# Kernel optimization log

Measured on AMD Instinct MI355X. Metric: run time of the kernel, lower is better.

Reference implementation:

```python
import jax, jax.numpy as jnp
import numpy as np

D_MODEL = 256
D_STATE = 64
NGROUPS = 2
EXPAND = 4
HEADDIM = 128
D_CONV = 4
D_INNER = EXPAND * D_MODEL              # 1024
NHEADS = D_INNER // HEADDIM             # 8
GN = NGROUPS * D_STATE                  # 128
D_IN_PROJ = 2 * D_INNER + 2 * GN + NHEADS  # 2312
EPS = 1e-5


def setup_inputs() -> dict:
    key = jax.random.key(0)
    ks = jax.random.split(key, 12)
    B, L = 2, 4096
    u = jax.random.normal(ks[0], (B, L, D_MODEL), dtype=jnp.float32)
    ln_gamma = jnp.ones((D_MODEL,), jnp.float32)
    ln_beta = jnp.zeros((D_MODEL,), jnp.float32)
    W_in = jax.random.normal(ks[1], (D_MODEL, D_IN_PROJ), jnp.float32) / np.sqrt(D_MODEL)
    conv_w = jax.random.normal(ks[2], (D_INNER + 2 * GN, D_CONV), jnp.float32) * 0.2
    conv_b = jax.random.normal(ks[3], (D_INNER + 2 * GN,), jnp.float32) * 0.02
    dt_bias = jnp.log(jnp.expm1(jax.random.uniform(ks[4], (NHEADS,), jnp.float32, 0.001, 0.1)))
    A_log = jnp.log(jax.random.uniform(ks[5], (NHEADS,), jnp.float32, 1.0, 16.0))
    D_param = jnp.ones((NHEADS,), jnp.float32)
    B_head_scale = jnp.ones((NHEADS, GN), jnp.float32) + 0.02 * jax.random.normal(ks[6], (NHEADS, GN), jnp.float32)
    rms_weight = jnp.ones((D_INNER,), jnp.float32)
    W_out = jax.random.normal(ks[7], (D_INNER, D_MODEL), jnp.float32) / np.sqrt(D_INNER)
    return dict(u=u, ln_gamma=ln_gamma, ln_beta=ln_beta, W_in=W_in, conv_w=conv_w,
                conv_b=conv_b, dt_bias=dt_bias, A_log=A_log, D_param=D_param,
                B_head_scale=B_head_scale, rms_weight=rms_weight, W_out=W_out)


def _mamba_mes(xn, W_in, conv_w, conv_b, dt_bias, A_log, D_param, B_head_scale, rms_weight, W_out):
    B, L, _ = xn.shape
    H, P, K = NHEADS, HEADDIM, D_CONV
    zxbcdt = xn @ W_in                                   # (B,L,2312)
    z = zxbcdt[..., :D_INNER]
    xBC = zxbcdt[..., D_INNER:D_INNER + D_INNER + 2 * GN]
    dt = zxbcdt[..., -H:]
    dt_pos = jax.nn.softplus(dt + dt_bias)               # (B,L,H)
    # causal depthwise conv1d + silu
    xp = jnp.pad(xBC, ((0, 0), (K - 1, 0), (0, 0)))
    conv = sum(xp[:, k:k + L, :] * conv_w[:, k] for k in range(K)) + conv_b
    xBC = jax.nn.silu(conv)
    x = xBC[..., :D_INNER]
    B_shared = xBC[..., D_INNER:D_INNER + GN]            # (B,L,GN)
    C_shared = xBC[..., D_INNER + GN:]                   # (B,L,GN)
    # MES: per-head B via diagonal scale, shared x (mean over heads) and shared C
    B_h = B_shared[:, :, None, :] * B_head_scale[None, None]          # (B,L,H,GN)
    x_shared = x.reshape(B, L, H, P).mean(axis=2)                     # (B,L,P)
    A = -jnp.exp(A_log)                                               # (H,)
    dA = jnp.exp(dt_pos * A)                                          # (B,L,H)
    # selective scan; per-head state (GN, P)
    def step(state, inp):
        dA_t, dt_t, B_t, C_t, x_t = inp   # (B,H),(B,H),(B,H,GN),(B,GN),(B,P)
        state = dA_t[:, :, None, None] * state + jnp.einsum('bh,bhn,bp->bhnp', dt_t, B_t, x_t)
        y_t = jnp.einsum('bn,bhnp->bhp', C_t, state)
        return state, y_t
    init = jnp.zeros((B, H, GN, P), xn.dtype)
    xs = (jnp.moveaxis(dA, 1, 0), jnp.moveaxis(dt_pos, 1, 0), jnp.moveaxis(B_h, 1, 0),
          jnp.moveaxis(C_shared, 1, 0), jnp.moveaxis(x_shared, 1, 0))
    _, ys = jax.lax.scan(step, init, xs)
    y = jnp.moveaxis(ys, 0, 1)                                        # (B,L,H,P)
    y = y + D_param[None, None, :, None] * x_shared[:, :, None, :]    # skip term D*x
    y = y.reshape(B, L, D_INNER)
    # gated RMSNorm: y * silu(z), then rmsnorm
    yg = y * jax.nn.silu(z)
    y = yg * jax.lax.rsqrt(jnp.mean(yg * yg, axis=-1, keepdims=True) + EPS) * rms_weight
    return y @ W_out


def reference(u, ln_gamma, ln_beta, W_in, conv_w, conv_b, dt_bias, A_log,
              D_param, B_head_scale, rms_weight, W_out):
    # pre-LayerNorm
    mu = jnp.mean(u, axis=-1, keepdims=True)
    var = jnp.mean((u - mu) ** 2, axis=-1, keepdims=True)
    xn = (u - mu) * jax.lax.rsqrt(var + EPS) * ln_gamma + ln_beta
    out = _mamba_mes(xn, W_in, conv_w, conv_b, dt_bias, A_log, D_param,
                     B_head_scale, rms_weight, W_out)
    return u + out  # dropout is identity in eval
```

## Files before the change

### kernel.cpp

```cpp
#include <hip/hip_runtime.h>
#include <math.h>

#define LN_TOK 4096
#define NB 2
#define NROWS (NB * LN_TOK)
#define DMODEL 256
#define DINNER 1024
#define NHEADS 8
#define GNN 128
#define DPROJ 2312
#define ZSTRIDE 2432
#define EPSF 1e-5f
#define NCHUNK 32
#define CHUNK 128
#define GPAD 72
#define TT 16

typedef unsigned short u16;
typedef unsigned int u32;
typedef __attribute__((ext_vector_type(8))) short shortx8;
typedef __attribute__((ext_vector_type(4))) float floatx4;

__device__ __forceinline__ float sigmoidf_(float v) { return 1.f / (1.f + __expf(-v)); }
__device__ __forceinline__ float siluf_(float v)    { return v / (1.f + __expf(-v)); }
__device__ __forceinline__ float softplusf_(float v){ return v > 20.f ? v : log1pf(__expf(v)); }
__device__ __forceinline__ float b2f(u16 h) { return __uint_as_float(((u32)h) << 16); }
__device__ __forceinline__ u16 f2b(float f) {
    u32 u = __float_as_uint(f);
    u32 r = (u + 0x7fffu + ((u >> 16) & 1u)) >> 16;
    return (u16)r;
}

__global__ void k_ln(const float* __restrict__ u, const float* __restrict__ gam,
                     const float* __restrict__ bet, u16* __restrict__ xn) {
    int row = blockIdx.x;
    int tid = threadIdx.x;
    float v = u[(size_t)row * DMODEL + tid];
    __shared__ float s1[256], s2[256];
    s1[tid] = v; s2[tid] = v * v;
    __syncthreads();
    for (int off = 128; off > 0; off >>= 1) {
        if (tid < off) { s1[tid] += s1[tid + off]; s2[tid] += s2[tid + off]; }
        __syncthreads();
    }
    float mean = s1[0] * (1.f / DMODEL);
    float var  = s2[0] * (1.f / DMODEL) - mean * mean;
    float r = rsqrtf(var + EPSF);
    xn[(size_t)row * DMODEL + tid] = f2b((v - mean) * r * gam[tid] + bet[tid]);
}

__global__ void k_tcast(const float* __restrict__ in, u16* __restrict__ out,
                        int R, int C, int Cp) {
    __shared__ float tile[64][65];
    int c0 = blockIdx.x * 64, r0 = blockIdx.y * 64;
    int tx = threadIdx.x & 63, ty = threadIdx.x >> 6;
    for (int rr = ty; rr < 64; rr += 4) {
        int r = r0 + rr, c = c0 + tx;
        tile[rr][tx] = (r < R && c < C) ? in[(size_t)r * C + c] : 0.f;
    }
    __syncthreads();
    for (int cc = ty; cc < 64; cc += 4) {
        int c = c0 + cc, r = r0 + tx;
        if (c < Cp && r < R) out[(size_t)c * R + r] = f2b(tile[tx][cc]);
    }
}

__global__ __launch_bounds__(256) void k_gemm_bf(const u16* __restrict__ A,
                                                 const u16* __restrict__ Bt,
                                                 u16* __restrict__ C,
                                                 int K, int ldc) {
    __shared__ u16 As[128 * GPAD];
    __shared__ u16 Bs[128 * GPAD];
    int tid = threadIdx.x;
    int wave = tid >> 6, lane = tid & 63;
    int wm = wave >> 1, wn = wave & 1;
    int quad = lane >> 4, l16 = lane & 15;
    int m0 = blockIdx.y * 128, n0 = blockIdx.x * 128;
    floatx4 acc[4][4] = {};
    for (int k0 = 0; k0 < K; k0 += 64) {
#pragma unroll
        for (int p = 0; p < 4; p++) {
            int i = p * 256 + tid;
            int row = i >> 3, kk = (i & 7) << 3;
            *(int4*)&As[row * GPAD + kk] = *(const int4*)&A[(size_t)(m0 + row) * K + k0 + kk];
            *(int4*)&Bs[row * GPAD + kk] = *(const int4*)&Bt[(size_t)(n0 + row) * K + k0 + kk];
        }
        __syncthreads();
#pragma unroll
        for (int ks = 0; ks < 64; ks += 32) {
            shortx8 af[4], bfr[4];
#pragma unroll
            for (int i = 0; i < 4; i++)
                af[i] = *(shortx8*)&As[(wm * 64 + i * 16 + l16) * GPAD + ks + (quad << 3)];
#pragma unroll
            for (int j = 0; j < 4; j++)
                bfr[j] = *(shortx8*)&Bs[(wn * 64 + j * 16 + l16) * GPAD + ks + (quad << 3)];
#pragma unroll
            for (int i = 0; i < 4; i++)
#pragma unroll
                for (int j = 0; j < 4; j++)
                    acc[i][j] = __builtin_amdgcn_mfma_f32_16x16x32_bf16(af[i], bfr[j], acc[i][j], 0, 0, 0);
        }
        __syncthreads();
    }
#pragma unroll
    for (int i = 0; i < 4; i++) {
        int row = m0 + wm * 64 + i * 16 + quad * 4;
#pragma unroll
        for (int j = 0; j < 4; j++) {
            int col = n0 + wn * 64 + j * 16 + l16;
#pragma unroll
            for (int r = 0; r < 4; r++)
                C[(size_t)(row + r) * ldc + col] = f2b(acc[i][j][r]);
        }
    }
}

__global__ __launch_bounds__(256) void k_gemm2(const u16* __restrict__ A,
                                               const u16* __restrict__ Bt,
                                               float* __restrict__ C,
                                               int K, int ldc,
                                               const float* __restrict__ addC) {
    __shared__ u16 As[128 * GPAD];
    __shared__ u16 Bs[64 * GPAD];
    int tid = threadIdx.x;
    int wave = tid >> 6, lane = tid & 63;
    int wm = wave >> 1, wn = wave & 1;
    int quad = lane >> 4, l16 = lane & 15;
    int m0 = blockIdx.y * 128, n0 = blockIdx.x * 64;
    floatx4 acc[4][2] = {};
    for (int k0 = 0; k0 < K; k0 += 64) {
#pragma unroll
        for (int p = 0; p < 4; p++) {
            int i = p * 256 + tid;
            int row = i >> 3, kk = (i & 7) << 3;
            *(int4*)&As[row * GPAD + kk] = *(const int4*)&A[(size_t)(m0 + row) * K + k0 + kk];
        }
#pragma unroll
        for (int p = 0; p < 2; p++) {
            int i = p * 256 + tid;
            int row = i >> 3, kk = (i & 7) << 3;
            *(int4*)&Bs[row * GPAD + kk] = *(const int4*)&Bt[(size_t)(n0 + row) * K + k0 + kk];
        }
        __syncthreads();
#pragma unroll
        for (int ks = 0; ks < 64; ks += 32) {
            shortx8 af[4], bfr[2];
#pragma unroll
            for (int i = 0; i < 4; i++)
                af[i] = *(shortx8*)&As[(wm * 64 + i * 16 + l16) * GPAD + ks + (quad << 3)];
#pragma unroll
            for (int j = 0; j < 2; j++)
                bfr[j] = *(shortx8*)&Bs[(wn * 32 + j * 16 + l16) * GPAD + ks + (quad << 3)];
#pragma unroll
            for (int i = 0; i < 4; i++)
#pragma unroll
                for (int j = 0; j < 2; j++)
                    acc[i][j] = __builtin_amdgcn_mfma_f32_16x16x32_bf16(af[i], bfr[j], acc[i][j], 0, 0, 0);
        }
        __syncthreads();
    }
#pragma unroll
    for (int i = 0; i < 4; i++) {
        int row = m0 + wm * 64 + i * 16 + quad * 4;
#pragma unroll
        for (int j = 0; j < 2; j++) {
            int col = n0 + wn * 32 + j * 16 + l16;
#pragma unroll
            for (int r = 0; r < 4; r++) {
                size_t idx = (size_t)(row + r) * ldc + col;
                float v = acc[i][j][r];
                if (addC) v += addC[idx];
                C[idx] = v;
            }
        }
    }
}

#define LDW 1296
__global__ __launch_bounds__(256) void k_conv(const u16* __restrict__ zxb,
                                              const float* __restrict__ cw,
                                              const float* __restrict__ cb,
                                              const float* __restrict__ dt_bias,
                                              const float* __restrict__ A_log,
                                              u16* __restrict__ xsh, u16* __restrict__ Bsh,
                                              u16* __restrict__ Csh, u16* __restrict__ XT,
                                              u16* __restrict__ BT,
                                              float* __restrict__ dtp, float* __restrict__ laa) {
    int blk = blockIdx.x;
    int b = blk / (LN_TOK / TT), tile = blk % (LN_TOK / TT);
    int t0 = tile * TT;
    int tid = threadIdx.x;
    __shared__ u16 ld[(TT + 3) * LDW];
    __shared__ float sv[TT][260];
    __shared__ u16 bcv[TT][132];

    for (int i = tid; i < (TT + 3) * 161; i += 256) {
        int r = i / 161, ch = (i % 161) * 8;
        int t = t0 - 3 + r;
        int4 v = make_int4(0, 0, 0, 0);
        if (t >= 0)
            v = *(const int4*)&zxb[((size_t)(b * LN_TOK + t)) * ZSTRIDE + DINNER + ch];
        *(int4*)&ld[r * LDW + ch] = v;
    }

    int cmap[5];
#pragma unroll
    for (int k = 0; k < 4; k++) cmap[k] = (tid >> 7) * 512 + (tid & 127) + 128 * k;
    cmap[4] = 1024 + tid;
    float w0[5], w1[5], w2[5], w3[5], bias[5];
#pragma unroll
    for (int k = 0; k < 5; k++) {
        int c = cmap[k];
        w0[k] = cw[c * 4 + 0]; w1[k] = cw[c * 4 + 1];
        w2[k] = cw[c * 4 + 2]; w3[k] = cw[c * 4 + 3];
        bias[k] = cb[c];
    }
    float dtb = 0.f, negA = 0.f;
    if (tid < NHEADS) { dtb = dt_bias[tid]; negA = -__expf(A_log[tid]); }

    __syncthreads();

    float h1[5], h2[5], h3[5];
#pragma unroll
    for (int k = 0; k < 5; k++) {
        h3[k] = b2f(ld[0 * LDW + cmap[k]]);
        h2[k] = b2f(ld[1 * LDW + cmap[k]]);
        h1[k] = b2f(ld[2 * LDW + cmap[k]]);
    }

    for (int m = 0; m < TT; m++) {
        int t = t0 + m;
        size_t rowp = (size_t)(b * LN_TOK + t) * GNN;
        float xpart = 0.f;
#pragma unroll
        for (int k = 0; k < 5; k++) {
            float cur = b2f(ld[(m + 3) * LDW + cmap[k]]);
            float conv = bias[k] + w3[k] * cur + w2[k] * h1[k] + w1[k] * h2[k] + w0[k] * h3[k];
            h3[k] = h2[k]; h2[k] = h1[k]; h1[k] = cur;
            float s = siluf_(conv);
            if (k < 4) xpart += s;
            else {
                u16 sb = f2b(s);
                if (tid < 128) { Bsh[rowp + tid] = sb; bcv[m][tid] = sb; }
                else           Csh[rowp + tid - 128] = sb;
            }
        }
        sv[m][tid] = xpart;
        if (tid < NHEADS) {
            float dtv = b2f(ld[(m + 3) * LDW + 1280 + tid]) + dtb;
            float dp = softplusf_(dtv);
            size_t idx = ((size_t)(b * NHEADS + tid)) * LN_TOK + t;
            dtp[idx] = dp;
            laa[idx] = negA * dp;
        }
    }
    __syncthreads();

    for (int idx = tid; idx < TT * 128; idx += 256) {
        int m = idx >> 7, p = idx & 127;
        xsh[(size_t)(b * LN_TOK + t0 + m) * GNN + p] =
            f2b((sv[m][p] + sv[m][p + 128]) * 0.125f);
    }
    {
        int p = tid & 127, tg = tid >> 7;
        u16 ox[8], ob[8];
#pragma unroll
        for (int j = 0; j < 8; j++) {
            int m = tg * 8 + j;
            ox[j] = f2b((sv[m][p] + sv[m][p + 128]) * 0.125f);
            ob[j] = bcv[m][p];
        }
        size_t base = ((size_t)(b * GNN + p)) * LN_TOK + t0 + tg * 8;
        int4 vx = make_int4((u32)ox[0] | ((u32)ox[1] << 16), (u32)ox[2] | ((u32)ox[3] << 16),
                            (u32)ox[4] | ((u32)ox[5] << 16), (u32)ox[6] | ((u32)ox[7] << 16));
        int4 vb = make_int4((u32)ob[0] | ((u32)ob[1] << 16), (u32)ob[2] | ((u32)ob[3] << 16),
                            (u32)ob[4] | ((u32)ob[5] << 16), (u32)ob[6] | ((u32)ob[7] << 16));
        *(int4*)&XT[base] = vx;
        *(int4*)&BT[base] = vb;
    }
}

__global__ void k_prefix(const float* __restrict__ laa, float* __restrict__ gcum) {
    int blk = blockIdx.x;
    int bh = blk / NCHUNK, c = blk % NCHUNK;
    int tid = threadIdx.x;
    __shared__ float s[128];
    size_t base = (size_t)bh * LN_TOK + c * CHUNK;
    s[tid] = laa[base + tid];
    __syncthreads();
    for (int off = 1; off < 128; off <<= 1) {
        float v = (tid >= off) ? s[tid - off] : 0.f;
        __syncthreads();
        s[tid] += v;
        __syncthreads();
    }
    gcum[base + tid] = s[tid];
}

__global__ __launch_bounds__(256) void k_chunkM(const u16* __restrict__ Bsh,
                                                const u16* __restrict__ Csh,
                                                const float* __restrict__ scale,
                                                const float* __restrict__ gcum,
                                                const float* __restrict__ dtp,
                                                u16* __restrict__ Mb) {
    int blk = blockIdx.x;
    int c = blk & 31, h = (blk >> 5) & 7, b = blk >> 8;
    int t0 = c * CHUNK;
    __shared__ u16 As[128 * GPAD];
    __shared__ u16 Bs[128 * GPAD];
    __shared__ float g[128], dts[128], sc[128];
    int tid = threadIdx.x;
    int wave = tid >> 6, lane = tid & 63;
    int wm = wave >> 1, wn = wave & 1;
    int quad = lane >> 4, l16 = lane & 15;
    size_t bhbase = (size_t)(b * NHEADS + h) * LN_TOK + t0;
    if (tid < 128) {
        g[tid] = gcum[bhbase + tid];
        dts[tid] = dtp[bhbase + tid];
        sc[tid] = scale[h * GNN + tid];
    }
    __syncthreads();
    floatx4 acc[4][4] = {};
    size_t rbase = (size_t)(b * LN_TOK + t0) * GNN;
    for (int k0 = 0; k0 < 128; k0 += 64) {
#pragma unroll
        for (int p = 0; p < 4; p++) {
            int i = p * 256 + tid;
            int row = i >> 3, kk = (i & 7) << 3;
            int4 raw = *(const int4*)&Bsh[rbase + (size_t)row * GNN + k0 + kk];
            u16* rp = (u16*)&raw;
            u32 w[4];
#pragma unroll
            for (int q = 0; q < 4; q++) {
                u16 a  = f2b(b2f(rp[2 * q])     * sc[k0 + kk + 2 * q]);
                u16 bb = f2b(b2f(rp[2 * q + 1]) * sc[k0 + kk + 2 * q + 1]);
                w[q] = (u32)a | ((u32)bb << 16);
            }
            *(int4*)&As[row * GPAD + kk] = make_int4(w[0], w[1], w[2], w[3]);
            *(int4*)&Bs[row * GPAD + kk] = *(const int4*)&Csh[rbase + (size_t)row * GNN + k0 + kk];
        }
        __syncthreads();
#pragma unroll
        for (int ks = 0; ks < 64; ks += 32) {
            shortx8 af[4], bfr[4];
#pragma unroll
            for (int i = 0; i < 4; i++)
                af[i] = *(shortx8*)&As[(wm * 64 + i * 16 + l16) * GPAD + ks + (quad << 3)];
#pragma unroll
            for (int j = 0; j < 4; j++)
                bfr[j] = *(shortx8*)&Bs[(wn * 64 + j * 16 + l16) * GPAD + ks + (quad << 3)];
#pragma unroll
            for (int i = 0; i < 4; i++)
#pragma unroll
                for (int j = 0; j < 4; j++)
                    acc[i][j] = __builtin_amdgcn_mfma_f32_16x16x32_bf16(af[i], bfr[j], acc[i][j], 0, 0, 0);
        }
        __syncthreads();
    }
    size_t mb = (size_t)blk * (CHUNK * CHUNK);
#pragma unroll
    for (int i = 0; i < 4; i++) {
        int s0 = wm * 64 + i * 16 + quad * 4;
#pragma unroll
        for (int j = 0; j < 4; j++) {
            int t = wn * 64 + j * 16 + l16;
            u16 o[4];
#pragma unroll
            for (int r = 0; r < 4; r++) {
                int s = s0 + r;
                float v = (s <= t) ? acc[i][j][r] * __expf(g[t] - g[s]) * dts[s] : 0.f;
                o[r] = f2b(v);
            }
            u32 lo = (u32)o[0] | ((u32)o[1] << 16);
            u32 hi = (u32)o[2] | ((u32)o[3] << 16);
            *(uint2*)&Mb[mb + (size_t)t * CHUNK + s0] = make_uint2(lo, hi);
        }
    }
}

__global__ __launch_bounds__(256) void k_chunkS(const u16* __restrict__ BT,
                                                const u16* __restrict__ XT,
                                                const float* __restrict__ scale,
                                                const float* __restrict__ gcum,
                                                const float* __restrict__ dtp,
                                                u16* __restrict__ states) {
    int blk = blockIdx.x;
    int c = blk & 31, h = (blk >> 5) & 7, b = blk >> 8;
    int t0 = c * CHUNK;
    __shared__ u16 As[128 * GPAD];
    __shared__ u16 Bs[128 * GPAD];
    __shared__ float esc[128], scl[128];
    int tid = threadIdx.x;
    int wave = tid >> 6, lane = tid & 63;
    int wm = wave >> 1, wn = wave & 1;
    int quad = lane >> 4, l16 = lane & 15;
    size_t bhbase = (size_t)(b * NHEADS + h) * LN_TOK + t0;
    if (tid < 128) {
        float gl = gcum[bhbase + 127];
        esc[tid] = __expf(gl - gcum[bhbase + tid]) * dtp[bhbase + tid];
        scl[tid] = scale[h * GNN + tid];
    }
    __syncthreads();
    floatx4 acc[4][4] = {};
    size_t tbase = (size_t)(b * GNN) * LN_TOK + t0;
    for (int k0 = 0; k0 < 128; k0 += 64) {
#pragma unroll
        for (int p = 0; p < 4; p++) {
            int i = p * 256 + tid;
            int row = i >> 3, kk = (i & 7) << 3;
            int4 raw = *(const int4*)&BT[tbase + (size_t)row * LN_TOK + k0 + kk];
            u16* rp = (u16*)&raw;
            float sr = scl[row];
            u32 w[4];
#pragma unroll
            for (int q = 0; q < 4; q++) {
                u16 a  = f2b(b2f(rp[2 * q])     * sr * esc[k0 + kk + 2 * q]);
                u16 bb = f2b(b2f(rp[2 * q + 1]) * sr * esc[k0 + kk + 2 * q + 1]);
                w[q] = (u32)a | ((u32)bb << 16);
            }
            *(int4*)&As[row * GPAD + kk] = make_int4(w[0], w[1], w[2], w[3]);
            *(int4*)&Bs[row * GPAD + kk] = *(const int4*)&XT[tbase + (size_t)row * LN_TOK + k0 + kk];
        }
        __syncthreads();
#pragma unroll
        for (int ks = 0; ks < 64; ks += 32) {
            shortx8 af[4], bfr[4];
#pragma unroll
            for (int i = 0; i < 4; i++)
                af[i] = *(shortx8*)&As[(wm * 64 + i * 16 + l16) * GPAD + ks + (quad << 3)];
#pragma unroll
            for (int j = 0; j < 4; j++)
                bfr[j] = *(shortx8*)&Bs[(wn * 64 + j * 16 + l16) * GPAD + ks + (quad << 3)];
#pragma unroll
            for (int i = 0; i < 4; i++)
#pragma unroll
                for (int j = 0; j < 4; j++)
                    acc[i][j] = __builtin_amdgcn_mfma_f32_16x16x32_bf16(af[i], bfr[j], acc[i][j], 0, 0, 0);
        }
        __syncthreads();
    }
    size_t sbase = (size_t)blk * 16384;
#pragma unroll
    for (int i = 0; i < 4; i++) {
        int n0 = wm * 64 + i * 16 + quad * 4;
#pragma unroll
        for (int j = 0; j < 4; j++) {
            int p = wn * 64 + j * 16 + l16;
            u16 o[4];
#pragma unroll
            for (int r = 0; r < 4; r++) o[r] = f2b(acc[i][j][r]);
            u32 lo = (u32)o[0] | ((u32)o[1] << 16);
            u32 hi = (u32)o[2] | ((u32)o[3] << 16);
            *(uint2*)&states[sbase + (size_t)p * CHUNK + n0] = make_uint2(lo, hi);
        }
    }
}

__global__ void k_scan(u16* __restrict__ states, const float* __restrict__ gcum) {
    int idx = blockIdx.x * 256 + threadIdx.x;
    int bh = idx >> 14;
    int np = idx & 16383;
    float run = 0.f;
    size_t base = (size_t)bh * NCHUNK * 16384 + np;
    size_t gb = (size_t)bh * LN_TOK;
    for (int c = 0; c < NCHUNK; c++) {
        float G = __expf(gcum[gb + c * CHUNK + 127]);
        float l = b2f(states[base + (size_t)c * 16384]);
        states[base + (size_t)c * 16384] = f2b(run);
        run = G * run + l;
    }
}

__global__ __launch_bounds__(256) void k_chunkY(const u16* __restrict__ Csh,
                                                const u16* __restrict__ states,
                                                const u16* __restrict__ Mb,
                                                const u16* __restrict__ XT,
                                                const float* __restrict__ gcum,
                                                u16* __restrict__ y) {
    int blk = blockIdx.x;
    int c = blk & 31, h = (blk >> 5) & 7, b = blk >> 8;
    int t0 = c * CHUNK;
    __shared__ u16 As[128 * GPAD];
    __shared__ u16 Bs[128 * GPAD];
    __shared__ float eg[128];
    int tid = threadIdx.x;
    int wave = tid >> 6, lane = tid & 63;
    int wm = wave >> 1, wn = wave & 1;
    int quad = lane >> 4, l16 = lane & 15;
    size_t bhbase = (size_t)(b * NHEADS + h) * LN_TOK + t0;
    if (tid < 128) eg[tid] = __expf(gcum[bhbase + tid]);
    __syncthreads();
    floatx4 acc[4][4] = {};
    size_t crow = (size_t)(b * LN_TOK + t0) * GNN;
    size_t sbase = (size_t)blk * 16384;
    size_t mbase = (size_t)blk * 16384;
    size_t xtb = (size_t)(b * GNN) * LN_TOK + t0;
    for (int k0 = 0; k0 < 128; k0 += 64) {
#pragma unroll
        for (int p = 0; p < 4; p++) {
            int i = p * 256 + tid;
            int row = i >> 3, kk = (i & 7) << 3;
            int4 raw = *(const int4*)&Csh[crow + (size_t)row * GNN + k0 + kk];
            float e = eg[row];
            u16* rp = (u16*)&raw;
            u32 w[4];
#pragma unroll
            for (int q = 0; q < 4; q++) {
                u16 a  = f2b(b2f(rp[2 * q]) * e);
                u16 bb = f2b(b2f(rp[2 * q + 1]) * e);
                w[q] = (u32)a | ((u32)bb << 16);
            }
            *(int4*)&As[row * GPAD + kk] = make_int4(w[0], w[1], w[2], w[3]);
            *(int4*)&Bs[row * GPAD + kk] = *(const int4*)&states[sbase + (size_t)row * CHUNK + k0 + kk];
        }
        __syncthreads();
#pragma unroll
        for (int ks = 0; ks < 64; ks += 32) {
            shortx8 af[4], bfr[4];
#pragma unroll
            for (int i = 0; i < 4; i++)
                af[i] = *(shortx8*)&As[(wm * 64 + i * 16 + l16) * GPAD + ks + (quad << 3)];
#pragma unroll
            for (int j = 0; j < 4; j++)
                bfr[j] = *(shortx8*)&Bs[(wn * 64 + j * 16 + l16) * GPAD + ks + (quad << 3)];
#pragma unroll
            for (int i = 0; i < 4; i++)
#pragma unroll
                for (int j = 0; j < 4; j++)
                    acc[i][j] = __builtin_amdgcn_mfma_f32_16x16x32_bf16(af[i], bfr[j], acc[i][j], 0, 0, 0);
        }
        __syncthreads();
    }
    for (int k0 = 0; k0 < 128; k0 += 64) {
#pragma unroll
        for (int p = 0; p < 4; p++) {
            int i = p * 256 + tid;
            int row = i >> 3, kk = (i & 7) << 3;
            *(int4*)&As[row * GPAD + kk] = *(const int4*)&Mb[mbase + (size_t)row * CHUNK + k0 + kk];
            *(int4*)&Bs[row * GPAD + kk] = *(const int4*)&XT[xtb + (size_t)row * LN_TOK + k0 + kk];
        }
        __syncthreads();
#pragma unroll
        for (int ks = 0; ks < 64; ks += 32) {
            shortx8 af[4], bfr[4];
#pragma unroll
            for (int i = 0; i < 4; i++)
                af[i] = *(shortx8*)&As[(wm * 64 + i * 16 + l16) * GPAD + ks + (quad << 3)];
#pragma unroll
            for (int j = 0; j < 4; j++)
                bfr[j] = *(shortx8*)&Bs[(wn * 64 + j * 16 + l16) * GPAD + ks + (quad << 3)];
#pragma unroll
            for (int i = 0; i < 4; i++)
#pragma unroll
                for (int j = 0; j < 4; j++)
                    acc[i][j] = __builtin_amdgcn_mfma_f32_16x16x32_bf16(af[i], bfr[j], acc[i][j], 0, 0, 0);
        }
        __syncthreads();
    }
#pragma unroll
    for (int i = 0; i < 4; i++) {
        int t = wm * 64 + i * 16 + quad * 4;
#pragma unroll
        for (int j = 0; j < 4; j++) {
            int p = wn * 64 + j * 16 + l16;
#pragma unroll
            for (int r = 0; r < 4; r++)
                y[((size_t)(b * LN_TOK + t0 + t + r)) * DINNER + h * GNN + p] = f2b(acc[i][j][r]);
        }
    }
}

__global__ void k_gate(const u16* __restrict__ y, const u16* __restrict__ zxb,
                       const u16* __restrict__ xsh, const float* __restrict__ Dp,
                       const float* __restrict__ rw, u16* __restrict__ ybuf) {
    int row = blockIdx.x;
    int tid = threadIdx.x;
    size_t yb = (size_t)row * DINNER;
    size_t zb = (size_t)row * ZSTRIDE;
    size_t xb = (size_t)row * GNN;
    float yg[4];
    float ss = 0.f;
#pragma unroll
    for (int q = 0; q < 4; q++) {
        int k = tid * 4 + q;
        int h = k >> 7, p = k & 127;
        float z = b2f(zxb[zb + k]);
        float v = (b2f(y[yb + k]) + Dp[h] * b2f(xsh[xb + p])) * z * sigmoidf_(z);
        yg[q] = v;
        ss += v * v;
    }
    __shared__ float red[256];
    red[tid] = ss;
    __syncthreads();
    for (int off = 128; off > 0; off >>= 1) {
        if (tid < off) red[tid] += red[tid + off];
        __syncthreads();
    }
    float scale = rsqrtf(red[0] * (1.f / DINNER) + EPSF);
#pragma unroll
    for (int q = 0; q < 4; q++) {
        int k = tid * 4 + q;
        ybuf[yb + k] = f2b(yg[q] * scale * rw[k]);
    }
}

extern "C" void kernel_launch(void* const* d_in, const int* in_sizes, int n_in,
                              void* d_out, int out_size, void* d_ws, size_t ws_size,
                              hipStream_t stream) {
    (void)in_sizes; (void)n_in; (void)out_size; (void)ws_size;
    const float* u        = (const float*)d_in[0];
    const float* ln_gamma = (const float*)d_in[1];
    const float* ln_beta  = (const float*)d_in[2];
    const float* W_in     = (const float*)d_in[3];
    const float* conv_w   = (const float*)d_in[4];
    const float* conv_b   = (const float*)d_in[5];
    const float* dt_bias  = (const float*)d_in[6];
    const float* A_log    = (const float*)d_in[7];
    const float* D_param  = (const float*)d_in[8];
    const float* B_scale  = (const float*)d_in[9];
    const float* rms_w    = (const float*)d_in[10];
    const float* W_out    = (const float*)d_in[11];
    float* out = (float*)d_out;

    char* ws = (char*)d_ws;
    u16*   xn_b   = (u16*)ws;                 ws += (size_t)NROWS * DMODEL * 2;
    u16*   Wt     = (u16*)ws;                 ws += (size_t)ZSTRIDE * DMODEL * 2;
    u16*   Wot    = (u16*)ws;                 ws += (size_t)DMODEL * DINNER * 2;
    u16*   zxb    = (u16*)ws;                 ws += (size_t)NROWS * ZSTRIDE * 2;
    u16*   xsh    = (u16*)ws;                 ws += (size_t)NROWS * GNN * 2;
    u16*   Bsh    = (u16*)ws;                 ws += (size_t)NROWS * GNN * 2;
    u16*   Csh    = (u16*)ws;                 ws += (size_t)NROWS * GNN * 2;
    u16*   XT     = (u16*)ws;                 ws += (size_t)NB * GNN * LN_TOK * 2;
    u16*   BT     = (u16*)ws;                 ws += (size_t)NB * GNN * LN_TOK * 2;
    float* dtp    = (float*)ws;               ws += (size_t)NB * NHEADS * LN_TOK * 4;
    float* laa    = (float*)ws;               ws += (size_t)NB * NHEADS * LN_TOK * 4;
    float* gcum   = (float*)ws;               ws += (size_t)NB * NHEADS * LN_TOK * 4;
    u16*   Mb     = (u16*)ws;                 ws += (size_t)512 * 16384 * 2;
    u16*   states = (u16*)ws;                 ws += (size_t)512 * 16384 * 2;
    u16*   ybig   = (u16*)ws;                 ws += (size_t)NROWS * DINNER * 2;
    u16*   ybuf   = Mb;

    k_ln<<<NROWS, 256, 0, stream>>>(u, ln_gamma, ln_beta, xn_b);

    k_tcast<<<dim3(ZSTRIDE / 64, DMODEL / 64), 256, 0, stream>>>(W_in, Wt, DMODEL, DPROJ, ZSTRIDE);
    k_tcast<<<dim3(DMODEL / 64, DINNER / 64), 256, 0, stream>>>(W_out, Wot, DINNER, DMODEL, DMODEL);

    k_gemm_bf<<<dim3(ZSTRIDE / 128, NROWS / 128), 256, 0, stream>>>(xn_b, Wt, zxb, DMODEL, ZSTRIDE);

    k_conv<<<NROWS / TT, 256, 0, stream>>>(zxb, conv_w, conv_b, dt_bias, A_log,
                                           xsh, Bsh, Csh, XT, BT, dtp, laa);

    k_prefix<<<NB * NHEADS * NCHUNK, 128, 0, stream>>>(laa, gcum);

    k_chunkM<<<NB * NHEADS * NCHUNK, 256, 0, stream>>>(Bsh, Csh, B_scale, gcum, dtp, Mb);

    k_chunkS<<<NB * NHEADS * NCHUNK, 256, 0, stream>>>(BT, XT, B_scale, gcum, dtp, states);

    k_scan<<<(NB * NHEADS * 16384) / 256, 256, 0, stream>>>(states, gcum);

    k_chunkY<<<NB * NHEADS * NCHUNK, 256, 0, stream>>>(Csh, states, Mb, XT, gcum, ybig);

    k_gate<<<NROWS, 256, 0, stream>>>(ybig, zxb, xsh, D_param, rms_w, ybuf);

    k_gemm2<<<dim3(DMODEL / 64, NROWS / 128), 256, 0, stream>>>(ybuf, Wot, out, DINNER, DMODEL, u);
}
```

Before: 224.5 us.

## Fuse chunk M and Y kernels, use global_load_lds in GEMMs, vectorize scan

```diff
diff --git a/kernel.cpp b/kernel.cpp
--- a/kernel.cpp
+++ b/kernel.cpp
@@ -13,7 +13,9 @@
 #define EPSF 1e-5f
 #define NCHUNK 32
 #define CHUNK 128
-#define GPAD 72
+#define APAD 72
+#define BPAD 64
+#define MPAD 136
 #define TT 16
 
 typedef unsigned short u16;
@@ -30,6 +32,10 @@
     u32 r = (u + 0x7fffu + ((u >> 16) & 1u)) >> 16;
     return (u16)r;
 }
+__device__ __forceinline__ void gld16(const void* g, void* l) {
+    __builtin_amdgcn_global_load_lds((const __attribute__((address_space(1))) unsigned int*)g,
+                                     (__attribute__((address_space(3))) unsigned int*)l, 16, 0, 0);
+}
 
 __global__ void k_ln(const float* __restrict__ u, const float* __restrict__ gam,
                      const float* __restrict__ bet, u16* __restrict__ xn) {
@@ -69,8 +75,8 @@
                                                  const u16* __restrict__ Bt,
                                                  u16* __restrict__ C,
                                                  int K, int ldc) {
-    __shared__ u16 As[128 * GPAD];
-    __shared__ u16 Bs[128 * GPAD];
+    __shared__ u16 As[128 * BPAD];
+    __shared__ u16 Bs[128 * BPAD];
     int tid = threadIdx.x;
     int wave = tid >> 6, lane = tid & 63;
     int wm = wave >> 1, wn = wave & 1;
@@ -82,8 +88,8 @@
         for (int p = 0; p < 4; p++) {
             int i = p * 256 + tid;
             int row = i >> 3, kk = (i & 7) << 3;
-            *(int4*)&As[row * GPAD + kk] = *(const int4*)&A[(size_t)(m0 + row) * K + k0 + kk];
-            *(int4*)&Bs[row * GPAD + kk] = *(const int4*)&Bt[(size_t)(n0 + row) * K + k0 + kk];
+            gld16(&A[(size_t)(m0 + row) * K + k0 + kk], &As[i * 8]);
+            gld16(&Bt[(size_t)(n0 + row) * K + k0 + kk], &Bs[i * 8]);
         }
         __syncthreads();
 #pragma unroll
@@ -91,10 +97,10 @@
             shortx8 af[4], bfr[4];
 #pragma unroll
             for (int i = 0; i < 4; i++)
-                af[i] = *(shortx8*)&As[(wm * 64 + i * 16 + l16) * GPAD + ks + (quad << 3)];
+                af[i] = *(shortx8*)&As[(wm * 64 + i * 16 + l16) * BPAD + ks + (quad << 3)];
 #pragma unroll
             for (int j = 0; j < 4; j++)
-                bfr[j] = *(shortx8*)&Bs[(wn * 64 + j * 16 + l16) * GPAD + ks + (quad << 3)];
+                bfr[j] = *(shortx8*)&Bs[(wn * 64 + j * 16 + l16) * BPAD + ks + (quad << 3)];
 #pragma unroll
             for (int i = 0; i < 4; i++)
 #pragma unroll
@@ -121,8 +127,8 @@
                                                float* __restrict__ C,
                                                int K, int ldc,
                                                const float* __restrict__ addC) {
-    __shared__ u16 As[128 * GPAD];
-    __shared__ u16 Bs[64 * GPAD];
+    __shared__ u16 As[128 * BPAD];
+    __shared__ u16 Bs[64 * BPAD];
     int tid = threadIdx.x;
     int wave = tid >> 6, lane = tid & 63;
     int wm = wave >> 1, wn = wave & 1;
@@ -134,13 +140,13 @@
         for (int p = 0; p < 4; p++) {
             int i = p * 256 + tid;
             int row = i >> 3, kk = (i & 7) << 3;
-            *(int4*)&As[row * GPAD + kk] = *(const int4*)&A[(size_t)(m0 + row) * K + k0 + kk];
+            gld16(&A[(size_t)(m0 + row) * K + k0 + kk], &As[i * 8]);
         }
 #pragma unroll
         for (int p = 0; p < 2; p++) {
             int i = p * 256 + tid;
             int row = i >> 3, kk = (i & 7) << 3;
-            *(int4*)&Bs[row * GPAD + kk] = *(const int4*)&Bt[(size_t)(n0 + row) * K + k0 + kk];
+            gld16(&Bt[(size_t)(n0 + row) * K + k0 + kk], &Bs[i * 8]);
         }
         __syncthreads();
 #pragma unroll
@@ -148,10 +154,10 @@
             shortx8 af[4], bfr[2];
 #pragma unroll
             for (int i = 0; i < 4; i++)
-                af[i] = *(shortx8*)&As[(wm * 64 + i * 16 + l16) * GPAD + ks + (quad << 3)];
+                af[i] = *(shortx8*)&As[(wm * 64 + i * 16 + l16) * BPAD + ks + (quad << 3)];
 #pragma unroll
             for (int j = 0; j < 2; j++)
-                bfr[j] = *(shortx8*)&Bs[(wn * 32 + j * 16 + l16) * GPAD + ks + (quad << 3)];
+                bfr[j] = *(shortx8*)&Bs[(wn * 32 + j * 16 + l16) * BPAD + ks + (quad << 3)];
 #pragma unroll
             for (int i = 0; i < 4; i++)
 #pragma unroll
@@ -298,87 +304,6 @@
     gcum[base + tid] = s[tid];
 }
 
-__global__ __launch_bounds__(256) void k_chunkM(const u16* __restrict__ Bsh,
-                                                const u16* __restrict__ Csh,
-                                                const float* __restrict__ scale,
-                                                const float* __restrict__ gcum,
-                                                const float* __restrict__ dtp,
-                                                u16* __restrict__ Mb) {
-    int blk = blockIdx.x;
-    int c = blk & 31, h = (blk >> 5) & 7, b = blk >> 8;
-    int t0 = c * CHUNK;
-    __shared__ u16 As[128 * GPAD];
-    __shared__ u16 Bs[128 * GPAD];
-    __shared__ float g[128], dts[128], sc[128];
-    int tid = threadIdx.x;
-    int wave = tid >> 6, lane = tid & 63;
-    int wm = wave >> 1, wn = wave & 1;
-    int quad = lane >> 4, l16 = lane & 15;
-    size_t bhbase = (size_t)(b * NHEADS + h) * LN_TOK + t0;
-    if (tid < 128) {
-        g[tid] = gcum[bhbase + tid];
-        dts[tid] = dtp[bhbase + tid];
-        sc[tid] = scale[h * GNN + tid];
-    }
-    __syncthreads();
-    floatx4 acc[4][4] = {};
-    size_t rbase = (size_t)(b * LN_TOK + t0) * GNN;
-    for (int k0 = 0; k0 < 128; k0 += 64) {
-#pragma unroll
-        for (int p = 0; p < 4; p++) {
-            int i = p * 256 + tid;
-            int row = i >> 3, kk = (i & 7) << 3;
-            int4 raw = *(const int4*)&Bsh[rbase + (size_t)row * GNN + k0 + kk];
-            u16* rp = (u16*)&raw;
-            u32 w[4];
-#pragma unroll
-            for (int q = 0; q < 4; q++) {
-                u16 a  = f2b(b2f(rp[2 * q])     * sc[k0 + kk + 2 * q]);
-                u16 bb = f2b(b2f(rp[2 * q + 1]) * sc[k0 + kk + 2 * q + 1]);
-                w[q] = (u32)a | ((u32)bb << 16);
-            }
-            *(int4*)&As[row * GPAD + kk] = make_int4(w[0], w[1], w[2], w[3]);
-            *(int4*)&Bs[row * GPAD + kk] = *(const int4*)&Csh[rbase + (size_t)row * GNN + k0 + kk];
-        }
-        __syncthreads();
-#pragma unroll
-        for (int ks = 0; ks < 64; ks += 32) {
-            shortx8 af[4], bfr[4];
-#pragma unroll
-            for (int i = 0; i < 4; i++)
-                af[i] = *(shortx8*)&As[(wm * 64 + i * 16 + l16) * GPAD + ks + (quad << 3)];
-#pragma unroll
-            for (int j = 0; j < 4; j++)
-                bfr[j] = *(shortx8*)&Bs[(wn * 64 + j * 16 + l16) * GPAD + ks + (quad << 3)];
-#pragma unroll
-            for (int i = 0; i < 4; i++)
-#pragma unroll
-                for (int j = 0; j < 4; j++)
-                    acc[i][j] = __builtin_amdgcn_mfma_f32_16x16x32_bf16(af[i], bfr[j], acc[i][j], 0, 0, 0);
-        }
-        __syncthreads();
-    }
-    size_t mb = (size_t)blk * (CHUNK * CHUNK);
-#pragma unroll
-    for (int i = 0; i < 4; i++) {
-        int s0 = wm * 64 + i * 16 + quad * 4;
-#pragma unroll
-        for (int j = 0; j < 4; j++) {
-            int t = wn * 64 + j * 16 + l16;
-            u16 o[4];
-#pragma unroll
-            for (int r = 0; r < 4; r++) {
-                int s = s0 + r;
-                float v = (s <= t) ? acc[i][j][r] * __expf(g[t] - g[s]) * dts[s] : 0.f;
-                o[r] = f2b(v);
-            }
-            u32 lo = (u32)o[0] | ((u32)o[1] << 16);
-            u32 hi = (u32)o[2] | ((u32)o[3] << 16);
-            *(uint2*)&Mb[mb + (size_t)t * CHUNK + s0] = make_uint2(lo, hi);
-        }
-    }
-}
-
 __global__ __launch_bounds__(256) void k_chunkS(const u16* __restrict__ BT,
                                                 const u16* __restrict__ XT,
                                                 const float* __restrict__ scale,
@@ -388,8 +313,8 @@
     int blk = blockIdx.x;
     int c = blk & 31, h = (blk >> 5) & 7, b = blk >> 8;
     int t0 = c * CHUNK;
-    __shared__ u16 As[128 * GPAD];
-    __shared__ u16 Bs[128 * GPAD];
+    __shared__ u16 As[128 * APAD];
+    __shared__ u16 Bs[128 * APAD];
     __shared__ float esc[128], scl[128];
     int tid = threadIdx.x;
     int wave = tid >> 6, lane = tid & 63;
@@ -419,8 +344,8 @@
                 u16 bb = f2b(b2f(rp[2 * q + 1]) * sr * esc[k0 + kk + 2 * q + 1]);
                 w[q] = (u32)a | ((u32)bb << 16);
             }
-            *(int4*)&As[row * GPAD + kk] = make_int4(w[0], w[1], w[2], w[3]);
-            *(int4*)&Bs[row * GPAD + kk] = *(const int4*)&XT[tbase + (size_t)row * LN_TOK + k0 + kk];
+            *(int4*)&As[row * APAD + kk] = make_int4(w[0], w[1], w[2], w[3]);
+            *(int4*)&Bs[row * APAD + kk] = *(const int4*)&XT[tbase + (size_t)row * LN_TOK + k0 + kk];
         }
         __syncthreads();
 #pragma unroll
@@ -428,10 +353,10 @@
             shortx8 af[4], bfr[4];
 #pragma unroll
             for (int i = 0; i < 4; i++)
-                af[i] = *(shortx8*)&As[(wm * 64 + i * 16 + l16) * GPAD + ks + (quad << 3)];
+                af[i] = *(shortx8*)&As[(wm * 64 + i * 16 + l16) * APAD + ks + (quad << 3)];
 #pragma unroll
             for (int j = 0; j < 4; j++)
-                bfr[j] = *(shortx8*)&Bs[(wn * 64 + j * 16 + l16) * GPAD + ks + (quad << 3)];
+                bfr[j] = *(shortx8*)&Bs[(wn * 64 + j * 16 + l16) * APAD + ks + (quad << 3)];
 #pragma unroll
             for (int i = 0; i < 4; i++)
 #pragma unroll
@@ -459,49 +384,116 @@
 
 __global__ void k_scan(u16* __restrict__ states, const float* __restrict__ gcum) {
     int idx = blockIdx.x * 256 + threadIdx.x;
-    int bh = idx >> 14;
-    int np = idx & 16383;
-    float run = 0.f;
+    int bh = idx >> 12;
+    int np = (idx & 4095) * 4;
+    float r0 = 0.f, r1 = 0.f, r2 = 0.f, r3 = 0.f;
     size_t base = (size_t)bh * NCHUNK * 16384 + np;
     size_t gb = (size_t)bh * LN_TOK;
     for (int c = 0; c < NCHUNK; c++) {
         float G = __expf(gcum[gb + c * CHUNK + 127]);
-        float l = b2f(states[base + (size_t)c * 16384]);
-        states[base + (size_t)c * 16384] = f2b(run);
-        run = G * run + l;
-    }
-}
-
-__global__ __launch_bounds__(256) void k_chunkY(const u16* __restrict__ Csh,
-                                                const u16* __restrict__ states,
-                                                const u16* __restrict__ Mb,
-                                                const u16* __restrict__ XT,
-                                                const float* __restrict__ gcum,
-                                                u16* __restrict__ y) {
+        uint2 v = *(uint2*)&states[base + (size_t)c * 16384];
+        float l0 = b2f((u16)(v.x & 0xffff)), l1 = b2f((u16)(v.x >> 16));
+        float l2 = b2f((u16)(v.y & 0xffff)), l3 = b2f((u16)(v.y >> 16));
+        uint2 o;
+        o.x = (u32)f2b(r0) | ((u32)f2b(r1) << 16);
+        o.y = (u32)f2b(r2) | ((u32)f2b(r3) << 16);
+        *(uint2*)&states[base + (size_t)c * 16384] = o;
+        r0 = G * r0 + l0; r1 = G * r1 + l1; r2 = G * r2 + l2; r3 = G * r3 + l3;
+    }
+}
+
+__global__ __launch_bounds__(256) void k_chunkMY(const u16* __restrict__ Bsh,
+                                                 const u16* __restrict__ Csh,
+                                                 const float* __restrict__ scale,
+                                                 const u16* __restrict__ states,
+                                                 const u16* __restrict__ XT,
+                                                 const float* __restrict__ gcum,
+                                                 const float* __restrict__ dtp,
+                                                 u16* __restrict__ y) {
     int blk = blockIdx.x;
     int c = blk & 31, h = (blk >> 5) & 7, b = blk >> 8;
     int t0 = c * CHUNK;
-    __shared__ u16 As[128 * GPAD];
-    __shared__ u16 Bs[128 * GPAD];
-    __shared__ float eg[128];
+    __shared__ u16 As[128 * APAD];
+    __shared__ u16 Bs[128 * APAD];
+    __shared__ u16 Mt[128 * MPAD];
+    __shared__ float g[128], dts[128], sc[128], eg[128];
     int tid = threadIdx.x;
     int wave = tid >> 6, lane = tid & 63;
     int wm = wave >> 1, wn = wave & 1;
     int quad = lane >> 4, l16 = lane & 15;
     size_t bhbase = (size_t)(b * NHEADS + h) * LN_TOK + t0;
-    if (tid < 128) eg[tid] = __expf(gcum[bhbase + tid]);
+    if (tid < 128) {
+        float gv = gcum[bhbase + tid];
+        g[tid] = gv;
+        eg[tid] = __expf(gv);
+        dts[tid] = dtp[bhbase + tid];
+        sc[tid] = scale[h * GNN + tid];
+    }
     __syncthreads();
     floatx4 acc[4][4] = {};
-    size_t crow = (size_t)(b * LN_TOK + t0) * GNN;
-    size_t sbase = (size_t)blk * 16384;
-    size_t mbase = (size_t)blk * 16384;
-    size_t xtb = (size_t)(b * GNN) * LN_TOK + t0;
+    size_t rbase = (size_t)(b * LN_TOK + t0) * GNN;
     for (int k0 = 0; k0 < 128; k0 += 64) {
 #pragma unroll
         for (int p = 0; p < 4; p++) {
             int i = p * 256 + tid;
             int row = i >> 3, kk = (i & 7) << 3;
-            int4 raw = *(const int4*)&Csh[crow + (size_t)row * GNN + k0 + kk];
+            int4 raw = *(const int4*)&Bsh[rbase + (size_t)row * GNN + k0 + kk];
+            u16* rp = (u16*)&raw;
+            u32 w[4];
+#pragma unroll
+            for (int q = 0; q < 4; q++) {
+                u16 a  = f2b(b2f(rp[2 * q])     * sc[k0 + kk + 2 * q]);
+                u16 bb = f2b(b2f(rp[2 * q + 1]) * sc[k0 + kk + 2 * q + 1]);
+                w[q] = (u32)a | ((u32)bb << 16);
+            }
+            *(int4*)&As[row * APAD + kk] = make_int4(w[0], w[1], w[2], w[3]);
+            *(int4*)&Bs[row * APAD + kk] = *(const int4*)&Csh[rbase + (size_t)row * GNN + k0 + kk];
+        }
+        __syncthreads();
+#pragma unroll
+        for (int ks = 0; ks < 64; ks += 32) {
+            shortx8 af[4], bfr[4];
+#pragma unroll
+            for (int i = 0; i < 4; i++)
+                af[i] = *(shortx8*)&As[(wm * 64 + i * 16 + l16) * APAD + ks + (quad << 3)];
+#pragma unroll
+            for (int j = 0; j < 4; j++)
+                bfr[j] = *(shortx8*)&Bs[(wn * 64 + j * 16 + l16) * APAD + ks + (quad << 3)];
+#pragma unroll
+            for (int i = 0; i < 4; i++)
+#pragma unroll
+                for (int j = 0; j < 4; j++)
+                    acc[i][j] = __builtin_amdgcn_mfma_f32_16x16x32_bf16(af[i], bfr[j], acc[i][j], 0, 0, 0);
+        }
+        __syncthreads();
+    }
+#pragma unroll
+    for (int i = 0; i < 4; i++) {
+        int s0 = wm * 64 + i * 16 + quad * 4;
+#pragma unroll
+        for (int j = 0; j < 4; j++) {
+            int t = wn * 64 + j * 16 + l16;
+            u16 o[4];
+#pragma unroll
+            for (int r = 0; r < 4; r++) {
+                int s = s0 + r;
+                float v = (s <= t) ? acc[i][j][r] * __expf(g[t] - g[s]) * dts[s] : 0.f;
+                o[r] = f2b(v);
+            }
+            u32 lo = (u32)o[0] | ((u32)o[1] << 16);
+            u32 hi = (u32)o[2] | ((u32)o[3] << 16);
+            *(uint2*)&Mt[t * MPAD + s0] = make_uint2(lo, hi);
+            acc[i][j] = (floatx4){0.f, 0.f, 0.f, 0.f};
+        }
+    }
+    __syncthreads();
+    size_t sbase = (size_t)blk * 16384;
+    for (int k0 = 0; k0 < 128; k0 += 64) {
+#pragma unroll
+        for (int p = 0; p < 4; p++) {
+            int i = p * 256 + tid;
+            int row = i >> 3, kk = (i & 7) << 3;
+            int4 raw = *(const int4*)&Csh[rbase + (size_t)row * GNN + k0 + kk];
             float e = eg[row];
             u16* rp = (u16*)&raw;
             u32 w[4];
@@ -511,8 +503,8 @@
                 u16 bb = f2b(b2f(rp[2 * q + 1]) * e);
                 w[q] = (u32)a | ((u32)bb << 16);
             }
-            *(int4*)&As[row * GPAD + kk] = make_int4(w[0], w[1], w[2], w[3]);
-            *(int4*)&Bs[row * GPAD + kk] = *(const int4*)&states[sbase + (size_t)row * CHUNK + k0 + kk];
+            *(int4*)&As[row * APAD + kk] = make_int4(w[0], w[1], w[2], w[3]);
+            *(int4*)&Bs[row * APAD + kk] = *(const int4*)&states[sbase + (size_t)row * CHUNK + k0 + kk];
         }
         __syncthreads();
 #pragma unroll
@@ -520,10 +512,10 @@
             shortx8 af[4], bfr[4];
 #pragma unroll
             for (int i = 0; i < 4; i++)
-                af[i] = *(shortx8*)&As[(wm * 64 + i * 16 + l16) * GPAD + ks + (quad << 3)];
+                af[i] = *(shortx8*)&As[(wm * 64 + i * 16 + l16) * APAD + ks + (quad << 3)];
 #pragma unroll
             for (int j = 0; j < 4; j++)
-                bfr[j] = *(shortx8*)&Bs[(wn * 64 + j * 16 + l16) * GPAD + ks + (quad << 3)];
+                bfr[j] = *(shortx8*)&Bs[(wn * 64 + j * 16 + l16) * APAD + ks + (quad << 3)];
 #pragma unroll
             for (int i = 0; i < 4; i++)
 #pragma unroll
@@ -532,13 +524,13 @@
         }
         __syncthreads();
     }
+    size_t xtb = (size_t)(b * GNN) * LN_TOK + t0;
     for (int k0 = 0; k0 < 128; k0 += 64) {
 #pragma unroll
         for (int p = 0; p < 4; p++) {
             int i = p * 256 + tid;
             int row = i >> 3, kk = (i & 7) << 3;
-            *(int4*)&As[row * GPAD + kk] = *(const int4*)&Mb[mbase + (size_t)row * CHUNK + k0 + kk];
-            *(int4*)&Bs[row * GPAD + kk] = *(const int4*)&XT[xtb + (size_t)row * LN_TOK + k0 + kk];
+            *(int4*)&Bs[row * APAD + kk] = *(const int4*)&XT[xtb + (size_t)row * LN_TOK + k0 + kk];
         }
         __syncthreads();
 #pragma unroll
@@ -546,10 +538,10 @@
             shortx8 af[4], bfr[4];
 #pragma unroll
             for (int i = 0; i < 4; i++)
-                af[i] = *(shortx8*)&As[(wm * 64 + i * 16 + l16) * GPAD + ks + (quad << 3)];
+                af[i] = *(shortx8*)&Mt[(wm * 64 + i * 16 + l16) * MPAD + k0 + ks + (quad << 3)];
 #pragma unroll
             for (int j = 0; j < 4; j++)
-                bfr[j] = *(shortx8*)&Bs[(wn * 64 + j * 16 + l16) * GPAD + ks + (quad << 3)];
+                bfr[j] = *(shortx8*)&Bs[(wn * 64 + j * 16 + l16) * APAD + ks + (quad << 3)];
 #pragma unroll
             for (int i = 0; i < 4; i++)
 #pragma unroll
@@ -636,10 +628,9 @@
     float* dtp    = (float*)ws;               ws += (size_t)NB * NHEADS * LN_TOK * 4;
     float* laa    = (float*)ws;               ws += (size_t)NB * NHEADS * LN_TOK * 4;
     float* gcum   = (float*)ws;               ws += (size_t)NB * NHEADS * LN_TOK * 4;
-    u16*   Mb     = (u16*)ws;                 ws += (size_t)512 * 16384 * 2;
     u16*   states = (u16*)ws;                 ws += (size_t)512 * 16384 * 2;
     u16*   ybig   = (u16*)ws;                 ws += (size_t)NROWS * DINNER * 2;
-    u16*   ybuf   = Mb;
+    u16*   ybuf   = (u16*)ws;                 ws += (size_t)NROWS * DINNER * 2;
 
     k_ln<<<NROWS, 256, 0, stream>>>(u, ln_gamma, ln_beta, xn_b);
 
@@ -653,13 +644,12 @@
 
     k_prefix<<<NB * NHEADS * NCHUNK, 128, 0, stream>>>(laa, gcum);
 
-    k_chunkM<<<NB * NHEADS * NCHUNK, 256, 0, stream>>>(Bsh, Csh, B_scale, gcum, dtp, Mb);
-
     k_chunkS<<<NB * NHEADS * NCHUNK, 256, 0, stream>>>(BT, XT, B_scale, gcum, dtp, states);
 
-    k_scan<<<(NB * NHEADS * 16384) / 256, 256, 0, stream>>>(states, gcum);
-
-    k_chunkY<<<NB * NHEADS * NCHUNK, 256, 0, stream>>>(Csh, states, Mb, XT, gcum, ybig);
+    k_scan<<<256, 256, 0, stream>>>(states, gcum);
+
+    k_chunkMY<<<NB * NHEADS * NCHUNK, 256, 0, stream>>>(Bsh, Csh, B_scale, states, XT,
+                                                        gcum, dtp, ybig);
 
     k_gate<<<NROWS, 256, 0, stream>>>(ybig, zxb, xsh, D_param, rms_w, ybuf);
 
```

New measurement: 226.8 us. Within noise of the previous version (+1.0%).
